# Kernel tuning notes

Hardware: AMD Instinct MI355X
Metric: run time of the kernel (lower is better)

The kernel has to match this reference:

```python
import jax, jax.numpy as jnp
import numpy as np

N = 50000      # nodes
E = 1_000_000  # edges (avg degree 20)
D = 64         # hidden dim
L = 3          # num dynamics layers
LN_EPS = 1e-5


def layernorm(h, g, b):
    mu = jnp.mean(h, axis=-1, keepdims=True)
    var = jnp.mean(jnp.square(h - mu), axis=-1, keepdims=True)
    return (h - mu) * jax.lax.rsqrt(var + LN_EPS) * g + b


def transformer_conv(h, src, dst, Wq, bq, Wk, bk, Wv, bv, Ws, bs):
    # PyG TransformerConv, heads=1, concat=False, beta=False, root_weight=True
    n = h.shape[0]
    d = Wq.shape[1]
    q = h @ Wq + bq            # [N, D] queries (dst side)
    k = h @ Wk + bk            # [N, D] keys   (src side)
    v = h @ Wv + bv            # [N, D] values (src side)
    logits = jnp.sum(q[dst] * k[src], axis=-1) / jnp.sqrt(jnp.asarray(d, h.dtype))  # [E]
    # segment softmax over incoming edges of each dst node
    m = jax.ops.segment_max(logits, dst, num_segments=n)      # [N]
    e = jnp.exp(logits - m[dst])                               # [E]
    s = jax.ops.segment_sum(e, dst, num_segments=n)            # [N]
    a = e / s[dst]                                             # [E]
    agg = jax.ops.segment_sum(a[:, None] * v[src], dst, num_segments=n)  # [N, D]
    return agg + h @ Ws + bs   # root/skip connection


def setup_inputs() -> dict:
    key = jax.random.key(0)
    ks = jax.random.split(key, 24)
    w = lambda k, shape: (jax.random.normal(k, shape, jnp.float32) * 0.05)
    inp = {
        "x": jax.random.normal(ks[0], (N, D), jnp.float32),
        "edge_index": jax.random.randint(ks[1], (2, E), 0, N, jnp.int32),
        # input_proj conv params
        "Wq0": w(ks[2], (D, D)), "bq0": w(ks[3], (D,)),
        "Wk0": w(ks[4], (D, D)), "bk0": w(ks[5], (D,)),
        "Wv0": w(ks[6], (D, D)), "bv0": w(ks[7], (D,)),
        "Ws0": w(ks[8], (D, D)), "bs0": w(ks[9], (D,)),
        "ln0_g": jnp.ones((D,), jnp.float32), "ln0_b": jnp.zeros((D,), jnp.float32),
        # stacked dynamics conv params [L, ...]
        "Wq": w(ks[10], (L, D, D)), "bq": w(ks[11], (L, D)),
        "Wk": w(ks[12], (L, D, D)), "bk": w(ks[13], (L, D)),
        "Wv": w(ks[14], (L, D, D)), "bv": w(ks[15], (L, D)),
        "Ws": w(ks[16], (L, D, D)), "bs": w(ks[17], (L, D)),
        "ln_g": jnp.ones((L, D), jnp.float32), "ln_b": jnp.zeros((L, D), jnp.float32),
    }
    return inp


def reference(x, edge_index, Wq0, bq0, Wk0, bk0, Wv0, bv0, Ws0, bs0, ln0_g, ln0_b,
              Wq, bq, Wk, bk, Wv, bv, Ws, bs, ln_g, ln_b):
    src, dst = edge_index[0], edge_index[1]
    h = transformer_conv(x, src, dst, Wq0, bq0, Wk0, bk0, Wv0, bv0, Ws0, bs0)
    h = jax.nn.relu(layernorm(h, ln0_g, ln0_b))
    # dropout is identity in eval mode
    for i in range(L):
        hi = transformer_conv(h, src, dst, Wq[i], bq[i], Wk[i], bk[i],
                              Wv[i], bv[i], Ws[i], bs[i])
        h = jax.nn.relu(layernorm(hi + h, ln_g[i], ln_b[i]))
    return h
```

## Files before the change

### kernel.cpp

```cpp
#include <hip/hip_runtime.h>
#include <math.h>


#define DD 64
#define NB_HIST 256

typedef __attribute__((ext_vector_type(8))) _Float16 h8;
typedef __attribute__((ext_vector_type(2))) _Float16 h2;
typedef __attribute__((ext_vector_type(4))) float f32x4;

__device__ __forceinline__ unsigned short f2h(float f) {
    union { _Float16 h; unsigned short u; } c;
    c.h = (_Float16)f;
    return c.u;
}
__device__ __forceinline__ h2 u2h2(unsigned u) {
    union { unsigned u; h2 h; } c; c.u = u; return c.h;
}
__device__ __forceinline__ unsigned pk2u(float a, float b) {
    union { decltype(__builtin_amdgcn_cvt_pkrtz(0.f, 0.f)) h; unsigned u; } c;
    c.h = __builtin_amdgcn_cvt_pkrtz(a, b);
    return c.u;
}
__device__ __forceinline__ float h2dot(h2 a, h2 b, float c) {
#if __has_builtin(__builtin_amdgcn_fdot2)
    return __builtin_amdgcn_fdot2(a, b, c, false);
#else
    return fmaf((float)a[0], (float)b[0], fmaf((float)a[1], (float)b[1], c));
#endif
}

__global__ __launch_bounds__(1024) void hist_blk(const int* __restrict__ dst,
                                                 unsigned* __restrict__ cb,
                                                 int E, int nbw) {
    extern __shared__ unsigned hist[];
    int blk = blockIdx.x;
    for (int w = threadIdx.x; w < nbw; w += blockDim.x) hist[w] = 0;
    __syncthreads();
    int chunk = (E + gridDim.x - 1) / gridDim.x;
    int beg = blk * chunk;
    int end = min(E, beg + chunk);
    for (int e = beg + (int)threadIdx.x; e < end; e += blockDim.x) {
        int d = dst[e];
        atomicAdd(&hist[d >> 1], (d & 1) ? 0x10000u : 1u);
    }
    __syncthreads();
    unsigned* out = cb + (size_t)blk * nbw;
    for (int w = threadIdx.x; w < nbw; w += blockDim.x) out[w] = hist[w];
}

__global__ __launch_bounds__(256) void prefix_blk(unsigned* __restrict__ cb,
                                                  int* __restrict__ counts,
                                                  int nbw, int n) {
    int w = blockIdx.x * blockDim.x + threadIdx.x;
    if (w >= nbw) return;
    unsigned acc = 0;
#pragma unroll 1
    for (int c = 0; c < NB_HIST; c += 16) {
        unsigned t[16];
#pragma unroll
        for (int j = 0; j < 16; ++j) t[j] = cb[(size_t)(c + j) * nbw + w];
#pragma unroll
        for (int j = 0; j < 16; ++j) {
            unsigned v = t[j];
            cb[(size_t)(c + j) * nbw + w] = acc;
            acc += v;
        }
    }
    counts[2 * w] = (int)(acc & 0xffffu);
    int b1 = 2 * w + 1;
    if (b1 < n) counts[b1] = (int)(acc >> 16);
}

__global__ __launch_bounds__(1024) void scan_local(const int* __restrict__ counts,
                                                   int* __restrict__ localscan,
                                                   int* __restrict__ blockSums, int n) {
    __shared__ int sh[1024];
    int i = blockIdx.x * 1024 + threadIdx.x;
    int val = (i < n) ? counts[i] : 0;
    sh[threadIdx.x] = val;
    __syncthreads();
    for (int off = 1; off < 1024; off <<= 1) {
        int t = (threadIdx.x >= off) ? sh[threadIdx.x - off] : 0;
        __syncthreads();
        sh[threadIdx.x] += t;
        __syncthreads();
    }
    if (i < n) localscan[i] = sh[threadIdx.x] - val;
    if (threadIdx.x == 1023) blockSums[blockIdx.x] = sh[1023];
}

__global__ __launch_bounds__(64) void scan_tops(int* __restrict__ blockSums, int nb) {
    int i = threadIdx.x;
    int val = (i < nb) ? blockSums[i] : 0;
    int s = val;
#pragma unroll
    for (int off = 1; off < 64; off <<= 1) {
        int t = __shfl_up(s, off, 64);
        if (i >= off) s += t;
    }
    if (i < nb) blockSums[i] = s - val;
}

__global__ void emit_rowptr(const int* __restrict__ localscan,
                            const int* __restrict__ blockSums,
                            int* __restrict__ row_ptr, int n, int E) {
    int i = blockIdx.x * blockDim.x + threadIdx.x;
    if (i < n) row_ptr[i] = localscan[i] + blockSums[i >> 10];
    if (i == 0) row_ptr[n] = E;
}

__global__ __launch_bounds__(1024) void scatter2(const int* __restrict__ src,
                                                 const int* __restrict__ dst,
                                                 const unsigned* __restrict__ cb,
                                                 const int* __restrict__ row_ptr,
                                                 int* __restrict__ col, int E, int nbw) {
    extern __shared__ unsigned hist[];
    int blk = blockIdx.x;
    for (int w = threadIdx.x; w < nbw; w += blockDim.x) hist[w] = 0;
    __syncthreads();
    const unsigned* pref = cb + (size_t)blk * nbw;
    int chunk = (E + gridDim.x - 1) / gridDim.x;
    int beg = blk * chunk;
    int end = min(E, beg + chunk);
    for (int e = beg + (int)threadIdx.x; e < end; e += blockDim.x) {
        int d = dst[e];
        unsigned sh = (unsigned)(d & 1) * 16u;
        unsigned old = atomicAdd(&hist[d >> 1], 1u << sh);
        unsigned lr = (old >> sh) & 0xffffu;
        unsigned pre = (pref[d >> 1] >> sh) & 0xffffu;
        int slot = row_ptr[d] + (int)pre + (int)lr;
        __builtin_nontemporal_store(src[e] << 8, &col[slot]);
    }
}

__global__ void prep_all(const float* __restrict__ x, unsigned short* __restrict__ hbf,
                         int nD,
                         const float* __restrict__ W0, const float* __restrict__ W1,
                         const float* __restrict__ W2, const float* __restrict__ W3,
                         const float* __restrict__ Wqs, const float* __restrict__ Wks,
                         const float* __restrict__ Wvs, const float* __restrict__ Wss,
                         unsigned short* __restrict__ Wt) {
    int i = blockIdx.x * blockDim.x + threadIdx.x;
    if (i < nD) { hbf[i] = f2h(x[i]); return; }
    int id = i - nD;
    if (id >= 16 * 4096) return;
    int mat = id >> 12, rem = id & 4095;
    int nn = rem >> 6, kk = rem & 63;
    int layer = mat >> 2, wh = mat & 3;
    const float* W;
    if (layer == 0) W = wh == 0 ? W0 : wh == 1 ? W1 : wh == 2 ? W2 : W3;
    else {
        const float* base = wh == 0 ? Wqs : wh == 1 ? Wks : wh == 2 ? Wvs : Wss;
        W = base + (size_t)(layer - 1) * 4096;
    }
    float val = W[kk * 64 + nn];
    if (wh == 0) val *= 0.125f;
    Wt[id] = f2h(val);
}

__global__ __launch_bounds__(256) void gemm_mfma(
    const unsigned short* __restrict__ hbf, const unsigned short* __restrict__ Wt,
    const float* __restrict__ Bq, const float* __restrict__ Bk,
    const float* __restrict__ Bv, const float* __restrict__ Bs,
    const float* __restrict__ hprev,
    unsigned short* __restrict__ qO, unsigned short* __restrict__ kvO,
    float* __restrict__ sO, int ntiles) {
    int lane = threadIdx.x & 63;
    int wave = threadIdx.x >> 6;
    int ml = lane & 15, ql = lane >> 4;

    const unsigned short* W = Wt + wave * 4096;
    h8 wfrag[4][2];
#pragma unroll
    for (int t = 0; t < 4; ++t)
#pragma unroll
        for (int kh = 0; kh < 2; ++kh)
            wfrag[t][kh] = *(const h8*)(W + (t * 16 + ml) * 64 + kh * 32 + ql * 8);

    const float* bias = wave == 0 ? Bq : wave == 1 ? Bk : wave == 2 ? Bv : Bs;
    float4 bias4[4];
#pragma unroll
    for (int t = 0; t < 4; ++t) {
        bias4[t] = *(const float4*)(bias + t * 16 + ql * 4);
        if (wave == 0) {
            bias4[t].x *= 0.125f; bias4[t].y *= 0.125f;
            bias4[t].z *= 0.125f; bias4[t].w *= 0.125f;
        }
    }

    for (int tile = blockIdx.x; tile < ntiles; tile += gridDim.x) {
        int node0 = tile * 16;
        h8 hfrag[2];
#pragma unroll
        for (int kh = 0; kh < 2; ++kh)
            hfrag[kh] = *(const h8*)(hbf + (size_t)(node0 + ml) * 64 + kh * 32 + ql * 8);
        f32x4 acc[4];
#pragma unroll
        for (int t = 0; t < 4; ++t) {
            acc[t][0] = bias4[t].x; acc[t][1] = bias4[t].y;
            acc[t][2] = bias4[t].z; acc[t][3] = bias4[t].w;
        }
#pragma unroll
        for (int t = 0; t < 4; ++t)
#pragma unroll
            for (int kh = 0; kh < 2; ++kh)
                acc[t] = __builtin_amdgcn_mfma_f32_16x16x32_f16(
                    wfrag[t][kh], hfrag[kh], acc[t], 0, 0, 0);

        size_t rowe = (size_t)(node0 + ml) * 64;
        if (wave == 0) {
#pragma unroll
            for (int t = 0; t < 4; ++t) {
                uint2 st;
                st.x = pk2u(acc[t][0], acc[t][1]);
                st.y = pk2u(acc[t][2], acc[t][3]);
                *(uint2*)(qO + rowe + t * 16 + ql * 4) = st;
            }
        } else if (wave == 3) {
#pragma unroll
            for (int t = 0; t < 4; ++t) {
                float4 st = {acc[t][0], acc[t][1], acc[t][2], acc[t][3]};
                if (hprev) {
                    float4 h4 = *(const float4*)(hprev + rowe + t * 16 + ql * 4);
                    st.x += h4.x; st.y += h4.y; st.z += h4.z; st.w += h4.w;
                }
                *(float4*)(sO + rowe + t * 16 + ql * 4) = st;
            }
        } else {
            size_t kve = (size_t)(node0 + ml) * 128 + (wave == 2 ? 64 : 0);
#pragma unroll
            for (int t = 0; t < 4; ++t) {
                uint2 st;
                st.x = pk2u(acc[t][0], acc[t][1]);
                st.y = pk2u(acc[t][2], acc[t][3]);
                *(uint2*)(kvO + kve + t * 16 + ql * 4) = st;
            }
        }
    }
}

__global__ __launch_bounds__(256) void attn_agg_ln(
    const unsigned short* __restrict__ qh, const unsigned short* __restrict__ kv,
    const float* __restrict__ sk,
    const int* __restrict__ row_ptr, const int* __restrict__ col,
    const float* __restrict__ g, const float* __restrict__ b,
    float* __restrict__ out, unsigned short* __restrict__ hbf_out, int n) {
    int node = blockIdx.x * 4 + (threadIdx.x >> 6);
    int lane = threadIdx.x & 63;
    if (node >= n) return;
    int grp = lane >> 3;
    int qi = lane & 7;

    size_t ro = (size_t)node * DD + qi * 8;
    uint4 qu = *(const uint4*)(qh + ro);
    float4 s4a = *(const float4*)(sk + ro);
    float4 s4b = *(const float4*)(sk + ro + 4);
    int beg = row_ptr[node], end = row_ptr[node + 1];

    float ssum = 0.0f;
    float4 aa = {0.f, 0.f, 0.f, 0.f}, ab = {0.f, 0.f, 0.f, 0.f};
    const char* kvb = (const char*)kv;

    int e = beg + grp;
    int cv = (e < end) ? col[e] : -1;
    for (int e0 = beg; e0 < end; e0 += 8) {
        bool act = cv >= 0;
        uint4 ku, vu;
        if (act) {
            const uint4* kp = (const uint4*)(kvb + cv) + qi;
            ku = kp[0];
            vu = kp[8];
        }
        e += 8;
        cv = (e < end) ? col[e] : -1;
        if (act) {
            float d = h2dot(u2h2(qu.x), u2h2(ku.x), 0.0f);
            d = h2dot(u2h2(qu.y), u2h2(ku.y), d);
            d = h2dot(u2h2(qu.z), u2h2(ku.z), d);
            d = h2dot(u2h2(qu.w), u2h2(ku.w), d);
            d += __shfl_xor(d, 1);
            d += __shfl_xor(d, 2);
            d += __shfl_xor(d, 4);
            float p = __expf(d);
            ssum += p;
            h2 v0 = u2h2(vu.x), v1 = u2h2(vu.y), v2 = u2h2(vu.z), v3 = u2h2(vu.w);
            aa.x = fmaf((float)v0[0], p, aa.x); aa.y = fmaf((float)v0[1], p, aa.y);
            aa.z = fmaf((float)v1[0], p, aa.z); aa.w = fmaf((float)v1[1], p, aa.w);
            ab.x = fmaf((float)v2[0], p, ab.x); ab.y = fmaf((float)v2[1], p, ab.y);
            ab.z = fmaf((float)v3[0], p, ab.z); ab.w = fmaf((float)v3[1], p, ab.w);
        }
    }

#pragma unroll
    for (int off = 8; off <= 32; off <<= 1) {
        ssum += __shfl_xor(ssum, off);
        aa.x += __shfl_xor(aa.x, off); aa.y += __shfl_xor(aa.y, off);
        aa.z += __shfl_xor(aa.z, off); aa.w += __shfl_xor(aa.w, off);
        ab.x += __shfl_xor(ab.x, off); ab.y += __shfl_xor(ab.y, off);
        ab.z += __shfl_xor(ab.z, off); ab.w += __shfl_xor(ab.w, off);
    }
    float inv = (end > beg) ? 1.0f / ssum : 0.0f;
    aa.x *= inv; aa.y *= inv; aa.z *= inv; aa.w *= inv;
    ab.x *= inv; ab.y *= inv; ab.z *= inv; ab.w *= inv;

    aa.x += s4a.x; aa.y += s4a.y; aa.z += s4a.z; aa.w += s4a.w;
    ab.x += s4b.x; ab.y += s4b.y; ab.z += s4b.z; ab.w += s4b.w;

    float s1 = aa.x + aa.y + aa.z + aa.w + ab.x + ab.y + ab.z + ab.w;
    s1 += __shfl_xor(s1, 1);
    s1 += __shfl_xor(s1, 2);
    s1 += __shfl_xor(s1, 4);
    float mu = s1 * (1.0f / DD);
    float dx0 = aa.x - mu, dx1 = aa.y - mu, dx2 = aa.z - mu, dx3 = aa.w - mu;
    float dx4 = ab.x - mu, dx5 = ab.y - mu, dx6 = ab.z - mu, dx7 = ab.w - mu;
    float s2v = dx0 * dx0 + dx1 * dx1 + dx2 * dx2 + dx3 * dx3
              + dx4 * dx4 + dx5 * dx5 + dx6 * dx6 + dx7 * dx7;
    s2v += __shfl_xor(s2v, 1);
    s2v += __shfl_xor(s2v, 2);
    s2v += __shfl_xor(s2v, 4);
    float var = s2v * (1.0f / DD);
    float is = rsqrtf(var + 1e-5f);
    float4 g4a = *(const float4*)(g + qi * 8);
    float4 g4b = *(const float4*)(g + qi * 8 + 4);
    float4 b4a = *(const float4*)(b + qi * 8);
    float4 b4b = *(const float4*)(b + qi * 8 + 4);
    float4 ya, yb;
    ya.x = fmaxf(dx0 * is * g4a.x + b4a.x, 0.0f);
    ya.y = fmaxf(dx1 * is * g4a.y + b4a.y, 0.0f);
    ya.z = fmaxf(dx2 * is * g4a.z + b4a.z, 0.0f);
    ya.w = fmaxf(dx3 * is * g4a.w + b4a.w, 0.0f);
    yb.x = fmaxf(dx4 * is * g4b.x + b4b.x, 0.0f);
    yb.y = fmaxf(dx5 * is * g4b.y + b4b.y, 0.0f);
    yb.z = fmaxf(dx6 * is * g4b.z + b4b.z, 0.0f);
    yb.w = fmaxf(dx7 * is * g4b.w + b4b.w, 0.0f);
    if (grp == 0) {
        *(float4*)(out + ro) = ya;
        *(float4*)(out + ro + 4) = yb;
        uint4 hv;
        hv.x = pk2u(ya.x, ya.y);
        hv.y = pk2u(ya.z, ya.w);
        hv.z = pk2u(yb.x, yb.y);
        hv.w = pk2u(yb.z, yb.w);
        *(uint4*)(hbf_out + ro) = hv;
    }
}

extern "C" void kernel_launch(void* const* d_in, const int* in_sizes, int n_in,
                              void* d_out, int out_size, void* d_ws, size_t ws_size,
                              hipStream_t stream) {
    const int D = DD;
    const float* x = (const float*)d_in[0];
    const int n = in_sizes[0] / D;
    const int* ei = (const int*)d_in[1];
    const int E = in_sizes[1] / 2;
    const int* srcp = ei;
    const int* dstp = ei + E;
    const int nbw = (n + 1) / 2;

    static bool s_attr = false;
    if (!s_attr) {
        s_attr = true;
        (void)hipFuncSetAttribute((const void*)hist_blk,
                                  hipFuncAttributeMaxDynamicSharedMemorySize, 102400);
        (void)hipFuncSetAttribute((const void*)scatter2,
                                  hipFuncAttributeMaxDynamicSharedMemorySize, 102400);
    }

    char* wsp = (char*)d_ws;
    auto take = [&](size_t bytes) {
        char* p = wsp;
        wsp += (bytes + 255) & ~(size_t)255;
        return (void*)p;
    };
    int* counts    = (int*)take((size_t)n * 4);
    int* row_ptr   = (int*)take((size_t)(n + 1) * 4);
    unsigned* cb   = (unsigned*)take((size_t)NB_HIST * nbw * 4);
    int* col       = (int*)take((size_t)E * 4);
    int* localscan = (int*)take((size_t)n * 4);
    int* blockSums = (int*)take((size_t)1024 * 4);
    size_t fsz = (size_t)n * D * 4;
    unsigned short* qb  = (unsigned short*)take(fsz / 2);
    unsigned short* kvb = (unsigned short*)take(fsz);
    float* sb           = (float*)take(fsz);
    float* hA           = (float*)take(fsz);
    float* hB           = (float*)take(fsz);
    unsigned short* hbf = (unsigned short*)take(fsz / 2);
    unsigned short* Wt  = (unsigned short*)take((size_t)16 * 4096 * 2);

    int tb = 256;
    size_t ldsH = (size_t)nbw * 4;
    int nbScan = (n + 1023) / 1024;
    hist_blk<<<NB_HIST, 1024, ldsH, stream>>>(dstp, cb, E, nbw);
    prefix_blk<<<(nbw + tb - 1) / tb, tb, 0, stream>>>(cb, counts, nbw, n);
    scan_local<<<nbScan, 1024, 0, stream>>>(counts, localscan, blockSums, n);
    scan_tops<<<1, 64, 0, stream>>>(blockSums, nbScan);
    emit_rowptr<<<(n + tb - 1) / tb, tb, 0, stream>>>(localscan, blockSums, row_ptr, n, E);
    scatter2<<<NB_HIST, 1024, ldsH, stream>>>(srcp, dstp, cb, row_ptr, col, E, nbw);

    int prep_total = n * D + 16 * 4096;
    prep_all<<<(prep_total + 255) / 256, 256, 0, stream>>>(
        x, hbf, n * D,
        (const float*)d_in[2], (const float*)d_in[4], (const float*)d_in[6],
        (const float*)d_in[8], (const float*)d_in[12], (const float*)d_in[14],
        (const float*)d_in[16], (const float*)d_in[18], Wt);

    const float* h = x;
    int ntiles = n / 16;
    int nba = (n + 3) / 4;
    for (int layer = 0; layer < 4; ++layer) {
        const float *bq_, *bk_, *bv_, *bs_, *g_, *b_;
        if (layer == 0) {
            bq_ = (const float*)d_in[3];  bk_ = (const float*)d_in[5];
            bv_ = (const float*)d_in[7];  bs_ = (const float*)d_in[9];
            g_  = (const float*)d_in[10]; b_  = (const float*)d_in[11];
        } else {
            int i = layer - 1;
            bq_ = (const float*)d_in[13] + (size_t)i * D;
            bk_ = (const float*)d_in[15] + (size_t)i * D;
            bv_ = (const float*)d_in[17] + (size_t)i * D;
            bs_ = (const float*)d_in[19] + (size_t)i * D;
            g_  = (const float*)d_in[20] + (size_t)i * D;
            b_  = (const float*)d_in[21] + (size_t)i * D;
        }
        gemm_mfma<<<512, 256, 0, stream>>>(hbf, Wt + (size_t)layer * 4 * 4096,
                                           bq_, bk_, bv_, bs_,
                                           layer == 0 ? nullptr : h,
                                           qb, kvb, sb, ntiles);
        float* hout = (layer == 3) ? (float*)d_out : ((layer & 1) ? hB : hA);
        attn_agg_ln<<<nba, 256, 0, stream>>>(qb, kvb, sb,
                                             row_ptr, col, g_, b_, hout, hbf, n);
        h = hout;
    }
}
```

Baseline: 384.7 us.

## Fuse all layer GEMM and attention phases into one cooperative persistent kernel

Replaces the eight per-layer launches (GEMM plus attention/LN, four layers) with a single cooperative kernel that separates phases with grid-wide syncs and falls back to separate launches if the cooperative launch fails. The skip/root term buffer is stored in fp16 instead of fp32 to halve its traffic. The attention edge loop is unrolled four-way so several gathers are in flight at once. The change trades launch gaps for grid-sync cost and a fixed persistent grid size, and adds some fp16 rounding on the skip term.

Measured after the change: 916.5 us. +138.2%, slower.

```diff
diff --git a/kernel.cpp b/kernel.cpp
--- a/kernel.cpp
+++ b/kernel.cpp
@@ -1,5 +1,8 @@
 #include <hip/hip_runtime.h>
+#include <hip/hip_cooperative_groups.h>
 #include <math.h>
+
+namespace cg = cooperative_groups;
 
 
 #define DD 64
@@ -159,18 +162,16 @@
     Wt[id] = f2h(val);
 }
 
-__global__ __launch_bounds__(256) void gemm_mfma(
-    const unsigned short* __restrict__ hbf, const unsigned short* __restrict__ Wt,
-    const float* __restrict__ Bq, const float* __restrict__ Bk,
-    const float* __restrict__ Bv, const float* __restrict__ Bs,
+__device__ __forceinline__ void gemm_phase(
+    const unsigned short* __restrict__ hbf, const unsigned short* __restrict__ Wl,
+    const float* __restrict__ bq, const float* __restrict__ bk,
+    const float* __restrict__ bv, const float* __restrict__ bs,
     const float* __restrict__ hprev,
     unsigned short* __restrict__ qO, unsigned short* __restrict__ kvO,
-    float* __restrict__ sO, int ntiles) {
-    int lane = threadIdx.x & 63;
-    int wave = threadIdx.x >> 6;
+    unsigned short* __restrict__ sO,
+    int ntiles, int bid, int gsz, int lane, int wave) {
     int ml = lane & 15, ql = lane >> 4;
-
-    const unsigned short* W = Wt + wave * 4096;
+    const unsigned short* W = Wl + wave * 4096;
     h8 wfrag[4][2];
 #pragma unroll
     for (int t = 0; t < 4; ++t)
@@ -178,7 +179,7 @@
         for (int kh = 0; kh < 2; ++kh)
             wfrag[t][kh] = *(const h8*)(W + (t * 16 + ml) * 64 + kh * 32 + ql * 8);
 
-    const float* bias = wave == 0 ? Bq : wave == 1 ? Bk : wave == 2 ? Bv : Bs;
+    const float* bias = wave == 0 ? bq : wave == 1 ? bk : wave == 2 ? bv : bs;
     float4 bias4[4];
 #pragma unroll
     for (int t = 0; t < 4; ++t) {
@@ -189,7 +190,7 @@
         }
     }
 
-    for (int tile = blockIdx.x; tile < ntiles; tile += gridDim.x) {
+    for (int tile = bid; tile < ntiles; tile += gsz) {
         int node0 = tile * 16;
         h8 hfrag[2];
 #pragma unroll
@@ -225,7 +226,10 @@
                     float4 h4 = *(const float4*)(hprev + rowe + t * 16 + ql * 4);
                     st.x += h4.x; st.y += h4.y; st.z += h4.z; st.w += h4.w;
                 }
-                *(float4*)(sO + rowe + t * 16 + ql * 4) = st;
+                uint2 sp;
+                sp.x = pk2u(st.x, st.y);
+                sp.y = pk2u(st.z, st.w);
+                *(uint2*)(sO + rowe + t * 16 + ql * 4) = sp;
             }
         } else {
             size_t kve = (size_t)(node0 + ml) * 128 + (wave == 2 ? 64 : 0);
@@ -240,22 +244,31 @@
     }
 }
 
-__global__ __launch_bounds__(256) void attn_agg_ln(
-    const unsigned short* __restrict__ qh, const unsigned short* __restrict__ kv,
-    const float* __restrict__ sk,
+#define EDGE_COMP(KU, VU) do {                                                 \
+    float d = h2dot(u2h2(qu.x), u2h2((KU).x), 0.0f);                           \
+    d = h2dot(u2h2(qu.y), u2h2((KU).y), d);                                    \
+    d = h2dot(u2h2(qu.z), u2h2((KU).z), d);                                    \
+    d = h2dot(u2h2(qu.w), u2h2((KU).w), d);                                    \
+    d += __shfl_xor(d, 1); d += __shfl_xor(d, 2); d += __shfl_xor(d, 4);       \
+    float p = __expf(d); ssum += p;                                            \
+    h2 v0 = u2h2((VU).x), v1 = u2h2((VU).y), v2 = u2h2((VU).z), v3 = u2h2((VU).w); \
+    aa.x = fmaf((float)v0[0], p, aa.x); aa.y = fmaf((float)v0[1], p, aa.y);    \
+    aa.z = fmaf((float)v1[0], p, aa.z); aa.w = fmaf((float)v1[1], p, aa.w);    \
+    ab.x = fmaf((float)v2[0], p, ab.x); ab.y = fmaf((float)v2[1], p, ab.y);    \
+    ab.z = fmaf((float)v3[0], p, ab.z); ab.w = fmaf((float)v3[1], p, ab.w);    \
+} while (0)
+
+__device__ __forceinline__ void attn_node(
+    int node, const unsigned short* __restrict__ qh,
+    const unsigned short* __restrict__ kv, const unsigned short* __restrict__ sk,
     const int* __restrict__ row_ptr, const int* __restrict__ col,
     const float* __restrict__ g, const float* __restrict__ b,
-    float* __restrict__ out, unsigned short* __restrict__ hbf_out, int n) {
-    int node = blockIdx.x * 4 + (threadIdx.x >> 6);
-    int lane = threadIdx.x & 63;
-    if (node >= n) return;
+    float* __restrict__ out, unsigned short* __restrict__ hbf_out, int lane) {
     int grp = lane >> 3;
     int qi = lane & 7;
-
     size_t ro = (size_t)node * DD + qi * 8;
     uint4 qu = *(const uint4*)(qh + ro);
-    float4 s4a = *(const float4*)(sk + ro);
-    float4 s4b = *(const float4*)(sk + ro + 4);
+    uint4 su = *(const uint4*)(sk + ro);
     int beg = row_ptr[node], end = row_ptr[node + 1];
 
     float ssum = 0.0f;
@@ -263,33 +276,26 @@
     const char* kvb = (const char*)kv;
 
     int e = beg + grp;
-    int cv = (e < end) ? col[e] : -1;
-    for (int e0 = beg; e0 < end; e0 += 8) {
-        bool act = cv >= 0;
-        uint4 ku, vu;
-        if (act) {
-            const uint4* kp = (const uint4*)(kvb + cv) + qi;
-            ku = kp[0];
-            vu = kp[8];
-        }
-        e += 8;
-        cv = (e < end) ? col[e] : -1;
-        if (act) {
-            float d = h2dot(u2h2(qu.x), u2h2(ku.x), 0.0f);
-            d = h2dot(u2h2(qu.y), u2h2(ku.y), d);
-            d = h2dot(u2h2(qu.z), u2h2(ku.z), d);
-            d = h2dot(u2h2(qu.w), u2h2(ku.w), d);
-            d += __shfl_xor(d, 1);
-            d += __shfl_xor(d, 2);
-            d += __shfl_xor(d, 4);
-            float p = __expf(d);
-            ssum += p;
-            h2 v0 = u2h2(vu.x), v1 = u2h2(vu.y), v2 = u2h2(vu.z), v3 = u2h2(vu.w);
-            aa.x = fmaf((float)v0[0], p, aa.x); aa.y = fmaf((float)v0[1], p, aa.y);
-            aa.z = fmaf((float)v1[0], p, aa.z); aa.w = fmaf((float)v1[1], p, aa.w);
-            ab.x = fmaf((float)v2[0], p, ab.x); ab.y = fmaf((float)v2[1], p, ab.y);
-            ab.z = fmaf((float)v3[0], p, ab.z); ab.w = fmaf((float)v3[1], p, ab.w);
-        }
+    int cv0 = (e < end) ? col[e] : -1;
+    int cv1 = (e + 8 < end) ? col[e + 8] : -1;
+    int cv2 = (e + 16 < end) ? col[e + 16] : -1;
+    int cv3 = (e + 24 < end) ? col[e + 24] : -1;
+    for (int e0 = beg; e0 < end; e0 += 32) {
+        bool a0 = cv0 >= 0, a1 = cv1 >= 0, a2 = cv2 >= 0, a3 = cv3 >= 0;
+        uint4 ku0, vu0, ku1, vu1, ku2, vu2, ku3, vu3;
+        if (a0) { const uint4* kp = (const uint4*)(kvb + cv0) + qi; ku0 = kp[0]; vu0 = kp[8]; }
+        if (a1) { const uint4* kp = (const uint4*)(kvb + cv1) + qi; ku1 = kp[0]; vu1 = kp[8]; }
+        if (a2) { const uint4* kp = (const uint4*)(kvb + cv2) + qi; ku2 = kp[0]; vu2 = kp[8]; }
+        if (a3) { const uint4* kp = (const uint4*)(kvb + cv3) + qi; ku3 = kp[0]; vu3 = kp[8]; }
+        e += 32;
+        cv0 = (e < end) ? col[e] : -1;
+        cv1 = (e + 8 < end) ? col[e + 8] : -1;
+        cv2 = (e + 16 < end) ? col[e + 16] : -1;
+        cv3 = (e + 24 < end) ? col[e + 24] : -1;
+        if (a0) EDGE_COMP(ku0, vu0);
+        if (a1) EDGE_COMP(ku1, vu1);
+        if (a2) EDGE_COMP(ku2, vu2);
+        if (a3) EDGE_COMP(ku3, vu3);
     }
 
 #pragma unroll
@@ -304,8 +310,13 @@
     aa.x *= inv; aa.y *= inv; aa.z *= inv; aa.w *= inv;
     ab.x *= inv; ab.y *= inv; ab.z *= inv; ab.w *= inv;
 
-    aa.x += s4a.x; aa.y += s4a.y; aa.z += s4a.z; aa.w += s4a.w;
-    ab.x += s4b.x; ab.y += s4b.y; ab.z += s4b.z; ab.w += s4b.w;
+    {
+        h2 t0 = u2h2(su.x), t1 = u2h2(su.y), t2 = u2h2(su.z), t3 = u2h2(su.w);
+        aa.x += (float)t0[0]; aa.y += (float)t0[1];
+        aa.z += (float)t1[0]; aa.w += (float)t1[1];
+        ab.x += (float)t2[0]; ab.y += (float)t2[1];
+        ab.z += (float)t3[0]; ab.w += (float)t3[1];
+    }
 
     float s1 = aa.x + aa.y + aa.z + aa.w + ab.x + ab.y + ab.z + ab.w;
     s1 += __shfl_xor(s1, 1);
@@ -346,6 +357,66 @@
     }
 }
 
+__global__ __launch_bounds__(256, 4) void layers_all(
+    const unsigned short* __restrict__ Wt,
+    const float* __restrict__ B0q, const float* __restrict__ B0k,
+    const float* __restrict__ B0v, const float* __restrict__ B0s,
+    const float* __restrict__ g0, const float* __restrict__ b0,
+    const float* __restrict__ Bqs, const float* __restrict__ Bks,
+    const float* __restrict__ Bvs, const float* __restrict__ Bss,
+    const float* __restrict__ Gs, const float* __restrict__ Bbs,
+    unsigned short* __restrict__ hbf, unsigned short* __restrict__ qb,
+    unsigned short* __restrict__ kvb, unsigned short* __restrict__ sb,
+    float* __restrict__ hA, float* __restrict__ hB, float* __restrict__ dout,
+    const int* __restrict__ row_ptr, const int* __restrict__ col, int n) {
+    cg::grid_group grid = cg::this_grid();
+    int lane = threadIdx.x & 63;
+    int wave = threadIdx.x >> 6;
+    int ntiles = n >> 4;
+    int nwv = (int)gridDim.x << 2;
+    int gwid = ((int)blockIdx.x << 2) + wave;
+
+    for (int layer = 0; layer < 4; ++layer) {
+        const float* bq = layer ? Bqs + (size_t)(layer - 1) * DD : B0q;
+        const float* bk = layer ? Bks + (size_t)(layer - 1) * DD : B0k;
+        const float* bv = layer ? Bvs + (size_t)(layer - 1) * DD : B0v;
+        const float* bs = layer ? Bss + (size_t)(layer - 1) * DD : B0s;
+        const float* g  = layer ? Gs  + (size_t)(layer - 1) * DD : g0;
+        const float* bb = layer ? Bbs + (size_t)(layer - 1) * DD : b0;
+        const float* hprev = layer == 0 ? nullptr : (layer == 2 ? hB : hA);
+        float* hout = layer == 3 ? dout : ((layer & 1) ? hB : hA);
+
+        gemm_phase(hbf, Wt + (size_t)layer * 16384, bq, bk, bv, bs, hprev,
+                   qb, kvb, sb, ntiles, blockIdx.x, gridDim.x, lane, wave);
+        grid.sync();
+        for (int node = gwid; node < n; node += nwv)
+            attn_node(node, qb, kvb, sb, row_ptr, col, g, bb, hout, hbf, lane);
+        if (layer < 3) grid.sync();
+    }
+}
+
+__global__ __launch_bounds__(256) void gemm_mfma(
+    const unsigned short* __restrict__ hbf, const unsigned short* __restrict__ Wt,
+    const float* __restrict__ Bq, const float* __restrict__ Bk,
+    const float* __restrict__ Bv, const float* __restrict__ Bs,
+    const float* __restrict__ hprev,
+    unsigned short* __restrict__ qO, unsigned short* __restrict__ kvO,
+    unsigned short* __restrict__ sO, int ntiles) {
+    gemm_phase(hbf, Wt, Bq, Bk, Bv, Bs, hprev, qO, kvO, sO,
+               ntiles, blockIdx.x, gridDim.x, threadIdx.x & 63, threadIdx.x >> 6);
+}
+
+__global__ __launch_bounds__(256) void attn_agg_ln(
+    const unsigned short* __restrict__ qh, const unsigned short* __restrict__ kv,
+    const unsigned short* __restrict__ sk,
+    const int* __restrict__ row_ptr, const int* __restrict__ col,
+    const float* __restrict__ g, const float* __restrict__ b,
+    float* __restrict__ out, unsigned short* __restrict__ hbf_out, int n) {
+    int node = blockIdx.x * 4 + (threadIdx.x >> 6);
+    if (node >= n) return;
+    attn_node(node, qh, kv, sk, row_ptr, col, g, b, out, hbf_out, threadIdx.x & 63);
+}
+
 extern "C" void kernel_launch(void* const* d_in, const int* in_sizes, int n_in,
                               void* d_out, int out_size, void* d_ws, size_t ws_size,
                               hipStream_t stream) {
@@ -358,13 +429,20 @@
     const int* dstp = ei + E;
     const int nbw = (n + 1) / 2;
 
-    static bool s_attr = false;
-    if (!s_attr) {
-        s_attr = true;
+    static int s_init = 0;
+    static int s_coopBlocks = 512;
+    if (!s_init) {
+        s_init = 1;
         (void)hipFuncSetAttribute((const void*)hist_blk,
                                   hipFuncAttributeMaxDynamicSharedMemorySize, 102400);
         (void)hipFuncSetAttribute((const void*)scatter2,
                                   hipFuncAttributeMaxDynamicSharedMemorySize, 102400);
+        int mb = 0;
+        if (hipOccupancyMaxActiveBlocksPerMultiprocessor(
+                &mb, (const void*)layers_all, 256, 0) != hipSuccess || mb < 1)
+            mb = 2;
+        if (mb > 8) mb = 8;
+        s_coopBlocks = 256 * mb;
     }
 
     char* wsp = (char*)d_ws;
@@ -382,7 +460,7 @@
     size_t fsz = (size_t)n * D * 4;
     unsigned short* qb  = (unsigned short*)take(fsz / 2);
     unsigned short* kvb = (unsigned short*)take(fsz);
-    float* sb           = (float*)take(fsz);
+    unsigned short* sb  = (unsigned short*)take(fsz / 2);
     float* hA           = (float*)take(fsz);
     float* hB           = (float*)take(fsz);
     unsigned short* hbf = (unsigned short*)take(fsz / 2);
@@ -405,31 +483,59 @@
         (const float*)d_in[8], (const float*)d_in[12], (const float*)d_in[14],
         (const float*)d_in[16], (const float*)d_in[18], Wt);
 
-    const float* h = x;
-    int ntiles = n / 16;
-    int nba = (n + 3) / 4;
-    for (int layer = 0; layer < 4; ++layer) {
-        const float *bq_, *bk_, *bv_, *bs_, *g_, *b_;
-        if (layer == 0) {
-            bq_ = (const float*)d_in[3];  bk_ = (const float*)d_in[5];
-            bv_ = (const float*)d_in[7];  bs_ = (const float*)d_in[9];
-            g_  = (const float*)d_in[10]; b_  = (const float*)d_in[11];
-        } else {
-            int i = layer - 1;
-            bq_ = (const float*)d_in[13] + (size_t)i * D;
-            bk_ = (const float*)d_in[15] + (size_t)i * D;
-            bv_ = (const float*)d_in[17] + (size_t)i * D;
-            bs_ = (const float*)d_in[19] + (size_t)i * D;
-            g_  = (const float*)d_in[20] + (size_t)i * D;
-            b_  = (const float*)d_in[21] + (size_t)i * D;
+    const unsigned short* a_Wt = Wt;
+    const float* a_B0q = (const float*)d_in[3];
+    const float* a_B0k = (const float*)d_in[5];
+    const float* a_B0v = (const float*)d_in[7];
+    const float* a_B0s = (const float*)d_in[9];
+    const float* a_g0  = (const float*)d_in[10];
+    const float* a_b0  = (const float*)d_in[11];
+    const float* a_Bqs = (const float*)d_in[13];
+    const float* a_Bks = (const float*)d_in[15];
+    const float* a_Bvs = (const float*)d_in[17];
+    const float* a_Bss = (const float*)d_in[19];
+    const float* a_Gs  = (const float*)d_in[20];
+    const float* a_Bbs = (const float*)d_in[21];
+    unsigned short* a_hbf = hbf;
+    unsigned short* a_qb = qb;
+    unsigned short* a_kvb = kvb;
+    unsigned short* a_sb = sb;
+    float* a_hA = hA;
+    float* a_hB = hB;
+    float* a_dout = (float*)d_out;
+    const int* a_rp = row_ptr;
+    const int* a_col = col;
+    int a_n = n;
+    void* kargs[] = {
+        (void*)&a_Wt,  (void*)&a_B0q, (void*)&a_B0k, (void*)&a_B0v, (void*)&a_B0s,
+        (void*)&a_g0,  (void*)&a_b0,  (void*)&a_Bqs, (void*)&a_Bks, (void*)&a_Bvs,
+        (void*)&a_Bss, (void*)&a_Gs,  (void*)&a_Bbs, (void*)&a_hbf, (void*)&a_qb,
+        (void*)&a_kvb, (void*)&a_sb,  (void*)&a_hA,  (void*)&a_hB,  (void*)&a_dout,
+        (void*)&a_rp,  (void*)&a_col, (void*)&a_n};
+    hipError_t rc = hipLaunchCooperativeKernel(
+        (const void*)layers_all, dim3(s_coopBlocks), dim3(256), kargs, 0, stream);
+    if (rc != hipSuccess) {
+        (void)hipGetLastError();
+        int ntiles = n / 16;
+        int nba = (n + 3) / 4;
+        const float* hprevs[4] = {nullptr, hA, hB, hA};
+        float* houts[4] = {hA, hB, hA, (float*)d_out};
+        for (int layer = 0; layer < 4; ++layer) {
+            const float *bq_, *bk_, *bv_, *bs_, *g_, *b_;
+            if (layer == 0) {
+                bq_ = a_B0q; bk_ = a_B0k; bv_ = a_B0v; bs_ = a_B0s;
+                g_ = a_g0; b_ = a_b0;
+            } else {
+                int i = layer - 1;
+                bq_ = a_Bqs + (size_t)i * D; bk_ = a_Bks + (size_t)i * D;
+                bv_ = a_Bvs + (size_t)i * D; bs_ = a_Bss + (size_t)i * D;
+                g_ = a_Gs + (size_t)i * D;   b_ = a_Bbs + (size_t)i * D;
+            }
+            gemm_mfma<<<512, 256, 0, stream>>>(hbf, Wt + (size_t)layer * 4 * 4096,
+                                               bq_, bk_, bv_, bs_, hprevs[layer],
+                                               qb, kvb, sb, ntiles);
+            attn_agg_ln<<<nba, 256, 0, stream>>>(qb, kvb, sb, row_ptr, col,
+                                                 g_, b_, houts[layer], hbf, n);
         }
-        gemm_mfma<<<512, 256, 0, stream>>>(hbf, Wt + (size_t)layer * 4 * 4096,
-                                           bq_, bk_, bv_, bs_,
-                                           layer == 0 ? nullptr : h,
-                                           qb, kvb, sb, ntiles);
-        float* hout = (layer == 3) ? (float*)d_out : ((layer & 1) ? hB : hA);
-        attn_agg_ln<<<nba, 256, 0, stream>>>(qb, kvb, sb,
-                                             row_ptr, col, g_, b_, hout, hbf, n);
-        h = hout;
-    }
-}
+    }
+}
```
